# Kernel tuning notes

Measured on AMD Instinct MI355X. Metric: run time of the kernel, lower is better.

## Reference

```python
import jax, jax.numpy as jnp
import numpy as np

WH, WW = 8, 8            # window_size
NUM_HEADS = 8
DIM = 256
CPB_HIDDEN = 512
N = WH * WW


def _make_coords_table():
    # [1, 2*WH-1, 2*WW-1, 2] log-spaced continuous relative coords (Swin-V2)
    h = np.arange(-(WH - 1), WH, dtype=np.float32)
    w = np.arange(-(WW - 1), WW, dtype=np.float32)
    gh, gw = np.meshgrid(h, w, indexing='ij')
    table = np.stack([gh, gw], axis=-1)[None]  # [1,2WH-1,2WW-1,2]
    table[..., 0] /= (WH - 1)
    table[..., 1] /= (WW - 1)
    table *= 8.0
    table = np.sign(table) * np.log2(np.abs(table) + 1.0) / np.log2(8.0)
    return jnp.asarray(table, dtype=jnp.float32)


def _make_rel_pos_index():
    ch = np.arange(WH)
    cw = np.arange(WW)
    coords = np.stack(np.meshgrid(ch, cw, indexing='ij'))   # [2,WH,WW]
    cf = coords.reshape(2, -1)                               # [2,N]
    rel = cf[:, :, None] - cf[:, None, :]                    # [2,N,N]
    rel = rel.transpose(1, 2, 0).astype(np.int32)            # [N,N,2]
    rel[..., 0] += WH - 1
    rel[..., 1] += WW - 1
    rel[..., 0] *= 2 * WW - 1
    return jnp.asarray(rel.sum(-1), dtype=jnp.int32)         # [N,N]


def setup_inputs() -> dict:
    key = jax.random.key(0)
    ks = jax.random.split(key, 8)
    B_ = 2048
    nW = 64
    x = jax.random.normal(ks[0], (B_, N, DIM), dtype=jnp.float32)
    mask = jnp.zeros((nW, N, N), dtype=jnp.float32)
    qkv_w = jax.random.normal(ks[1], (3 * DIM, DIM), dtype=jnp.float32) * 0.02
    q_bias = jnp.zeros((DIM,), dtype=jnp.float32)
    v_bias = jnp.zeros((DIM,), dtype=jnp.float32)
    logit_scale = jnp.log(10.0 * jnp.ones((NUM_HEADS, 1, 1), dtype=jnp.float32))
    cpb_w1 = jax.random.normal(ks[2], (CPB_HIDDEN, 2), dtype=jnp.float32) * 0.02
    cpb_b1 = jnp.zeros((CPB_HIDDEN,), dtype=jnp.float32)
    cpb_w2 = jax.random.normal(ks[3], (NUM_HEADS, CPB_HIDDEN), dtype=jnp.float32) * 0.02
    proj_w = jax.random.normal(ks[4], (DIM, DIM), dtype=jnp.float32) * 0.02
    proj_b = jnp.zeros((DIM,), dtype=jnp.float32)
    return {
        'x': x, 'mask': mask,
        'qkv_w': qkv_w, 'q_bias': q_bias, 'v_bias': v_bias,
        'logit_scale': logit_scale,
        'cpb_w1': cpb_w1, 'cpb_b1': cpb_b1, 'cpb_w2': cpb_w2,
        'proj_w': proj_w, 'proj_b': proj_b,
        'coords_table': _make_coords_table(),
        'rel_idx': _make_rel_pos_index(),
    }


def reference(x, mask, qkv_w, q_bias, v_bias, logit_scale,
              cpb_w1, cpb_b1, cpb_w2, proj_w, proj_b,
              coords_table, rel_idx):
    B_, n, C = x.shape
    H = NUM_HEADS
    hd = C // H

    # qkv with [q_bias, 0, v_bias]
    qkv_bias = jnp.concatenate([q_bias, jnp.zeros_like(v_bias), v_bias])
    qkv = x @ qkv_w.T + qkv_bias                         # [B,N,3C]
    qkv = qkv.reshape(B_, n, 3, H, hd).transpose(2, 0, 3, 1, 4)
    q, k, v = qkv[0], qkv[1], qkv[2]                     # [B,H,N,hd]

    # cosine attention: L2-normalized q,k (eps as in F.normalize)
    qn = q / jnp.maximum(jnp.linalg.norm(q, axis=-1, keepdims=True), 1e-12)
    kn = k / jnp.maximum(jnp.linalg.norm(k, axis=-1, keepdims=True), 1e-12)
    attn = jnp.einsum('bhnd,bhmd->bhnm', qn, kn)         # [B,H,N,N]

    max_log = jnp.log(jnp.asarray(1.0 / 0.01, dtype=x.dtype))
    scale = jnp.exp(jnp.minimum(logit_scale, max_log))   # [H,1,1]
    attn = attn * scale

    # MLP relative position bias: 2 -> 512 -> H, gather, 16*sigmoid
    hid = jax.nn.relu(coords_table @ cpb_w1.T + cpb_b1)  # [1,2WH-1,2WW-1,512]
    table = (hid @ cpb_w2.T).reshape(-1, H)              # [(2WH-1)(2WW-1), H]
    bias = table[rel_idx.reshape(-1)].reshape(n, n, H)
    bias = 16.0 * jax.nn.sigmoid(bias.transpose(2, 0, 1))  # [H,N,N]
    attn = attn + bias[None]

    nW = mask.shape[0]
    attn = attn.reshape(B_ // nW, nW, H, n, n) + mask[None, :, None]
    attn = attn.reshape(B_, H, n, n)
    attn = jax.nn.softmax(attn, axis=-1)

    out = jnp.einsum('bhnm,bhmd->bhnd', attn, v)         # [B,H,N,hd]
    out = out.transpose(0, 2, 1, 3).reshape(B_, n, C)
    return out @ proj_w.T + proj_b
```

## Files before the change

### kernel.cpp

```cpp
#include <hip/hip_runtime.h>
#include <hip/hip_bf16.h>

typedef unsigned short u16;
typedef unsigned int   u32;
typedef __attribute__((ext_vector_type(8))) short short8;
typedef __attribute__((ext_vector_type(4))) short short4v;
typedef __attribute__((ext_vector_type(4))) float f32x4;

__device__ __forceinline__ u16 f2bf(float f) {
  u32 u = __float_as_uint(f);
  u32 r = (u + 0x7fffu + ((u >> 16) & 1u)) >> 16;
  return (u16)r;
}

__global__ __launch_bounds__(256) void wcvt_kernel(
    const float* __restrict__ qkvw, const float* __restrict__ pw,
    u16* __restrict__ wq, u16* __restrict__ wp) {
  const int e = (blockIdx.x * 256 + threadIdx.x) * 4;
  if (e < 196608) {
    const float4 v = *(const float4*)(qkvw + e);
    short4v o; o[0]=(short)f2bf(v.x); o[1]=(short)f2bf(v.y);
    o[2]=(short)f2bf(v.z); o[3]=(short)f2bf(v.w);
    *(short4v*)(wq + e) = o;
  } else {
    const int e2 = e - 196608;
    const float4 v = *(const float4*)(pw + e2);
    short4v o; o[0]=(short)f2bf(v.x); o[1]=(short)f2bf(v.y);
    o[2]=(short)f2bf(v.z); o[3]=(short)f2bf(v.w);
    *(short4v*)(wp + e2) = o;
  }
}

__global__ __launch_bounds__(256) void cpb_kernel(
    const float* __restrict__ ct, const float* __restrict__ w1,
    const float* __restrict__ b1, const float* __restrict__ w2,
    float* __restrict__ table) {
  const int r = blockIdx.x;
  const int t = threadIdx.x;
  const int lane = t & 63, wave = t >> 6;
  const float c0 = ct[r * 2 + 0];
  const float c1 = ct[r * 2 + 1];
  float acc[8] = {0.f, 0.f, 0.f, 0.f, 0.f, 0.f, 0.f, 0.f};
  for (int j = t; j < 512; j += 256) {
    float hid = fmaxf(c0 * w1[j * 2] + c1 * w1[j * 2 + 1] + b1[j], 0.f);
#pragma unroll
    for (int hh = 0; hh < 8; ++hh) acc[hh] += hid * w2[hh * 512 + j];
  }
#pragma unroll
  for (int hh = 0; hh < 8; ++hh)
#pragma unroll
    for (int off = 1; off < 64; off <<= 1) acc[hh] += __shfl_xor(acc[hh], off);
  __shared__ float red[4][8];
  if (lane == 0)
#pragma unroll
    for (int hh = 0; hh < 8; ++hh) red[wave][hh] = acc[hh];
  __syncthreads();
  if (t < 8) table[r * 8 + t] = red[0][t] + red[1][t] + red[2][t] + red[3][t];
}

__global__ __launch_bounds__(256) void bm_kernel(
    const float* __restrict__ table, const int* __restrict__ rel,
    const float* __restrict__ mask, float* __restrict__ bmP) {
  const int g = blockIdx.x * 256 + threadIdx.x;
  const int w = g >> 13;
  const int h = (g >> 10) & 7;
  const int m = (g >> 4) & 63;
  const int l = g & 15;
  float4 o;
#pragma unroll
  for (int j = 0; j < 4; ++j) {
    const int c = j * 16 + l;
    const float t = table[rel[m * 64 + c] * 8 + h];
    o[j] = 16.f / (1.f + __expf(-t)) + mask[(size_t)w * 4096 + m * 64 + c];
  }
  *(float4*)(bmP + ((((size_t)w * 8 + h) * 64 + m) * 64 + l * 4)) = o;
}

__global__ __launch_bounds__(512, 2) void fused_kernel(
    const float* __restrict__ X,
    const float* __restrict__ bmP,
    const float* __restrict__ lsc,
    const u16*  __restrict__ Wqb,
    const float* __restrict__ qb, const float* __restrict__ vbias,
    const u16*  __restrict__ Wpb,
    const float* __restrict__ pb,
    float* __restrict__ out) {
  __shared__ __attribute__((aligned(16))) u16 sA[16896];
  __shared__ __attribute__((aligned(16))) u16 sW[8][6912];

  const int bw = blockIdx.x;
  const int w  = bw & 63;
  const int tid  = threadIdx.x;
  const int wave = tid >> 6, lane = tid & 63;
  const int l15 = lane & 15, l4 = lane >> 4;
  const int h = wave;

  {
    const int cq  = tid & 7;
    const int rlo = tid >> 3;
    const float* xrow = X + ((size_t)bw * 64 + rlo) * 256;
#pragma unroll
    for (int kf = 0; kf < 8; ++kf) {
      const float4 xv = *(const float4*)(xrow + kf * 32 + cq * 4);
      short4v t4; t4[0]=(short)f2bf(xv.x); t4[1]=(short)f2bf(xv.y);
      t4[2]=(short)f2bf(xv.z); t4[3]=(short)f2bf(xv.w);
      *(short4v*)&sA[kf * 2048 + rlo * 32 + cq * 4] = t4;
    }
  }
  __syncthreads();

  u16* vt   = &sW[wave][0];
  u16* pbuf = &sW[wave][2304];

  f32x4 oa[4][2];

  {
    const int rb[6] = {h * 32, h * 32 + 16, 256 + h * 32, 256 + h * 32 + 16,
                       512 + h * 32, 512 + h * 32 + 16};
    f32x4 acc[4][6];
#pragma unroll
    for (int mi = 0; mi < 4; ++mi)
#pragma unroll
      for (int nj = 0; nj < 6; ++nj) acc[mi][nj] = (f32x4){0.f, 0.f, 0.f, 0.f};

    short8 bf_cur[6];
#pragma unroll
    for (int nj = 0; nj < 6; ++nj)
      bf_cur[nj] = *(const short8*)(Wqb + (size_t)(rb[nj] + l15) * 256 + l4 * 8);

#pragma unroll
    for (int kf = 0; kf < 8; ++kf) {
      short8 af[4];
#pragma unroll
      for (int mi = 0; mi < 4; ++mi)
        af[mi] = *(const short8*)&sA[kf * 2048 + (mi * 16 + l15) * 32 + l4 * 8];
      short8 bf_nxt[6];
      if (kf < 7) {
#pragma unroll
        for (int nj = 0; nj < 6; ++nj)
          bf_nxt[nj] = *(const short8*)(Wqb + (size_t)(rb[nj] + l15) * 256 + (kf + 1) * 32 + l4 * 8);
      }
#pragma unroll
      for (int nj = 0; nj < 6; ++nj)
#pragma unroll
        for (int mi = 0; mi < 4; ++mi)
          acc[mi][nj] = __builtin_amdgcn_mfma_f32_16x16x32_bf16(af[mi], bf_cur[nj], acc[mi][nj], 0, 0, 0);
      if (kf < 7) {
#pragma unroll
        for (int nj = 0; nj < 6; ++nj) bf_cur[nj] = bf_nxt[nj];
      }
    }

    u16* qstage = pbuf;
    u16* kstage = pbuf + 2048;
    {
      const float qb0 = qb[h * 32 + l15];
      const float qb1 = qb[h * 32 + 16 + l15];
#pragma unroll
      for (int mi = 0; mi < 4; ++mi)
#pragma unroll
        for (int r = 0; r < 4; ++r) {
          const float v0 = acc[mi][0][r] + qb0;
          const float v1 = acc[mi][1][r] + qb1;
          float ss = v0 * v0 + v1 * v1;
          ss += __shfl_xor(ss, 1); ss += __shfl_xor(ss, 2);
          ss += __shfl_xor(ss, 4); ss += __shfl_xor(ss, 8);
          const float inv = 1.f / fmaxf(sqrtf(ss), 1e-12f);
          const int m = mi * 16 + l4 * 4 + r;
          qstage[m * 32 + l15]      = f2bf(v0 * inv);
          qstage[m * 32 + 16 + l15] = f2bf(v1 * inv);
        }
#pragma unroll
      for (int mi = 0; mi < 4; ++mi)
#pragma unroll
        for (int r = 0; r < 4; ++r) {
          const float v0 = acc[mi][2][r];
          const float v1 = acc[mi][3][r];
          float ss = v0 * v0 + v1 * v1;
          ss += __shfl_xor(ss, 1); ss += __shfl_xor(ss, 2);
          ss += __shfl_xor(ss, 4); ss += __shfl_xor(ss, 8);
          const float inv = 1.f / fmaxf(sqrtf(ss), 1e-12f);
          const int m = mi * 16 + l4 * 4 + r;
          kstage[m * 32 + l15]      = f2bf(v0 * inv);
          kstage[m * 32 + 16 + l15] = f2bf(v1 * inv);
        }
      const float vb0 = vbias[h * 32 + l15];
      const float vb1 = vbias[h * 32 + 16 + l15];
#pragma unroll
      for (int mi = 0; mi < 4; ++mi)
#pragma unroll
        for (int r = 0; r < 4; ++r) {
          const int m = mi * 16 + l4 * 4 + r;
          vt[l15 * 72 + m]        = f2bf(acc[mi][4][r] + vb0);
          vt[(16 + l15) * 72 + m] = f2bf(acc[mi][5][r] + vb1);
        }
    }

    const float* bmbase = bmP + (((size_t)(w * 8 + h)) * 64) * 64 + l15 * 4;
    float4 bmv[4][4];
#pragma unroll
    for (int i = 0; i < 4; ++i)
#pragma unroll
      for (int r = 0; r < 4; ++r) {
        const int m = i * 16 + l4 * 4 + r;
        bmv[i][r] = *(const float4*)(bmbase + (size_t)m * 64);
      }

    short8 aq[4], bk[4];
#pragma unroll
    for (int i = 0; i < 4; ++i)
      aq[i] = *(const short8*)&qstage[(i * 16 + l15) * 32 + l4 * 8];
#pragma unroll
    for (int j = 0; j < 4; ++j)
      bk[j] = *(const short8*)&kstage[(j * 16 + l15) * 32 + l4 * 8];

    f32x4 s[4][4];
    __builtin_amdgcn_s_setprio(1);
#pragma unroll
    for (int i = 0; i < 4; ++i)
#pragma unroll
      for (int j = 0; j < 4; ++j) {
        const f32x4 z = {0.f, 0.f, 0.f, 0.f};
        s[i][j] = __builtin_amdgcn_mfma_f32_16x16x32_bf16(aq[i], bk[j], z, 0, 0, 0);
      }
    __builtin_amdgcn_s_setprio(0);

    const float scale = __expf(fminf(lsc[h], 4.60517018598809136804f));
    u16* pW = pbuf;

#pragma unroll
    for (int i = 0; i < 4; ++i)
#pragma unroll
      for (int r = 0; r < 4; ++r) {
        const int m = i * 16 + l4 * 4 + r;
        float v0[4]; float mx = -3.0e38f;
#pragma unroll
        for (int j = 0; j < 4; ++j) {
          const float sv = s[i][j][r] * scale + bmv[i][r][j];
          v0[j] = sv; mx = fmaxf(mx, sv);
        }
        mx = fmaxf(mx, __shfl_xor(mx, 1)); mx = fmaxf(mx, __shfl_xor(mx, 2));
        mx = fmaxf(mx, __shfl_xor(mx, 4)); mx = fmaxf(mx, __shfl_xor(mx, 8));
        float sum = 0.f;
#pragma unroll
        for (int j = 0; j < 4; ++j) { v0[j] = __expf(v0[j] - mx); sum += v0[j]; }
        sum += __shfl_xor(sum, 1); sum += __shfl_xor(sum, 2);
        sum += __shfl_xor(sum, 4); sum += __shfl_xor(sum, 8);
        const float isum = 1.f / sum;
#pragma unroll
        for (int j = 0; j < 4; ++j)
          pW[m * 72 + j * 16 + l15] = f2bf(v0[j] * isum);
      }

#pragma unroll
    for (int i = 0; i < 4; ++i)
#pragma unroll
      for (int nb = 0; nb < 2; ++nb) oa[i][nb] = (f32x4){0.f, 0.f, 0.f, 0.f};
#pragma unroll
    for (int kb = 0; kb < 2; ++kb) {
      short8 pa[4];
#pragma unroll
      for (int i = 0; i < 4; ++i)
        pa[i] = *(const short8*)&pW[(i * 16 + l15) * 72 + kb * 32 + l4 * 8];
      __builtin_amdgcn_s_setprio(1);
#pragma unroll
      for (int nb = 0; nb < 2; ++nb) {
        const short8 vb8 = *(const short8*)&vt[(nb * 16 + l15) * 72 + kb * 32 + l4 * 8];
#pragma unroll
        for (int i = 0; i < 4; ++i)
          oa[i][nb] = __builtin_amdgcn_mfma_f32_16x16x32_bf16(pa[i], vb8, oa[i][nb], 0, 0, 0);
      }
      __builtin_amdgcn_s_setprio(0);
    }
  }

  __syncthreads();

#pragma unroll
  for (int i = 0; i < 4; ++i)
#pragma unroll
    for (int nb = 0; nb < 2; ++nb)
#pragma unroll
      for (int r = 0; r < 4; ++r) {
        const int m = i * 16 + l4 * 4 + r;
        sA[m * 264 + h * 32 + nb * 16 + l15] = f2bf(oa[i][nb][r]);
      }
  __syncthreads();

  {
    const int n0 = wave * 32;
    const u16* pbase = Wpb + (size_t)(n0 + l15) * 256 + l4 * 8;
    f32x4 pacc[4][2];
#pragma unroll
    for (int mi = 0; mi < 4; ++mi)
#pragma unroll
      for (int nj = 0; nj < 2; ++nj) pacc[mi][nj] = (f32x4){0.f, 0.f, 0.f, 0.f};

    short8 bfr_cur[2];
#pragma unroll
    for (int nj = 0; nj < 2; ++nj)
      bfr_cur[nj] = *(const short8*)(pbase + (size_t)(nj * 16) * 256);

#pragma unroll
    for (int ks = 0; ks < 8; ++ks) {
      const int k0 = ks * 32;
      short8 afr[4];
#pragma unroll
      for (int mi = 0; mi < 4; ++mi)
        afr[mi] = *(const short8*)&sA[(mi * 16 + l15) * 264 + k0 + l4 * 8];
      short8 bfr_nxt[2];
      if (ks < 7) {
#pragma unroll
        for (int nj = 0; nj < 2; ++nj)
          bfr_nxt[nj] = *(const short8*)(pbase + (size_t)(nj * 16) * 256 + k0 + 32);
      }
#pragma unroll
      for (int nj = 0; nj < 2; ++nj)
#pragma unroll
        for (int mi = 0; mi < 4; ++mi)
          pacc[mi][nj] = __builtin_amdgcn_mfma_f32_16x16x32_bf16(afr[mi], bfr_cur[nj], pacc[mi][nj], 0, 0, 0);
      if (ks < 7) {
#pragma unroll
        for (int nj = 0; nj < 2; ++nj) bfr_cur[nj] = bfr_nxt[nj];
      }
    }
    float* orow = out + (size_t)bw * 64 * 256;
#pragma unroll
    for (int mi = 0; mi < 4; ++mi)
#pragma unroll
      for (int nj = 0; nj < 2; ++nj) {
        const int n = n0 + nj * 16 + l15;
        const float bias = pb[n];
#pragma unroll
        for (int r = 0; r < 4; ++r) {
          const int m = mi * 16 + l4 * 4 + r;
          orow[(size_t)m * 256 + n] = pacc[mi][nj][r] + bias;
        }
      }
  }
}

extern "C" void kernel_launch(void* const* d_in, const int* in_sizes, int n_in,
                              void* d_out, int out_size, void* d_ws, size_t ws_size,
                              hipStream_t stream) {
  (void)in_sizes; (void)n_in; (void)out_size; (void)ws_size;
  const float* x    = (const float*)d_in[0];
  const float* mask = (const float*)d_in[1];
  const float* qkvw = (const float*)d_in[2];
  const float* qb   = (const float*)d_in[3];
  const float* vb   = (const float*)d_in[4];
  const float* lsc  = (const float*)d_in[5];
  const float* w1   = (const float*)d_in[6];
  const float* b1   = (const float*)d_in[7];
  const float* w2   = (const float*)d_in[8];
  const float* pw   = (const float*)d_in[9];
  const float* pb   = (const float*)d_in[10];
  const float* ct   = (const float*)d_in[11];
  const int* rel    = (const int*)d_in[12];
  float* out = (float*)d_out;

  char* ws = (char*)d_ws;
  float* table = (float*)(ws);
  u16* Wqb = (u16*)(ws + 262144);
  u16* Wpb = (u16*)(ws + 720896);
  float* bmP = (float*)(ws + (1 << 20));

  wcvt_kernel<<<256, 256, 0, stream>>>(qkvw, pw, Wqb, Wpb);
  cpb_kernel<<<225, 256, 0, stream>>>(ct, w1, b1, w2, table);
  bm_kernel<<<2048, 256, 0, stream>>>(table, rel, mask, bmP);
  fused_kernel<<<2048, 512, 0, stream>>>(x, bmP, lsc, Wqb, qb, vb,
                                         Wpb, pb, out);
}
```

Before: 472.9 us.

## Split each head across two waves with 1024-thread blocks in fused attention

Doubles the fused kernel's block size to 1024 threads so two waves share each head. One wave computes Q plus half of V and the other computes K plus the other half, then each takes half the query rows for scores, softmax, PV and the output projection. The aim is to cut per-wave register pressure and serial work and raise parallelism per window. In exchange it adds block-wide barriers between phases, reuses the Q staging buffer for P, and drops the explicit two-blocks-per-CU occupancy hint.

```diff
diff --git a/kernel.cpp b/kernel.cpp
--- a/kernel.cpp
+++ b/kernel.cpp
@@ -76,7 +76,7 @@
   *(float4*)(bmP + ((((size_t)w * 8 + h) * 64 + m) * 64 + l * 4)) = o;
 }
 
-__global__ __launch_bounds__(512, 2) void fused_kernel(
+__global__ __launch_bounds__(1024) void fused_kernel(
     const float* __restrict__ X,
     const float* __restrict__ bmP,
     const float* __restrict__ lsc,
@@ -93,40 +93,48 @@
   const int tid  = threadIdx.x;
   const int wave = tid >> 6, lane = tid & 63;
   const int l15 = lane & 15, l4 = lane >> 4;
-  const int h = wave;
-
-  {
-    const int cq  = tid & 7;
-    const int rlo = tid >> 3;
-    const float* xrow = X + ((size_t)bw * 64 + rlo) * 256;
-#pragma unroll
-    for (int kf = 0; kf < 8; ++kf) {
-      const float4 xv = *(const float4*)(xrow + kf * 32 + cq * 4);
+  const int h    = wave >> 1;
+  const int half = wave & 1;
+
+  {
+    const int row = tid >> 4;
+    const int c4  = tid & 15;
+    const float* xrow = X + ((size_t)bw * 64 + row) * 256;
+#pragma unroll
+    for (int u = 0; u < 4; ++u) {
+      const int col = u * 64 + c4 * 4;
+      const int kf = col >> 5, co = col & 31;
+      const float4 xv = *(const float4*)(xrow + col);
       short4v t4; t4[0]=(short)f2bf(xv.x); t4[1]=(short)f2bf(xv.y);
       t4[2]=(short)f2bf(xv.z); t4[3]=(short)f2bf(xv.w);
-      *(short4v*)&sA[kf * 2048 + rlo * 32 + cq * 4] = t4;
-    }
-  }
-  __syncthreads();
-
-  u16* vt   = &sW[wave][0];
-  u16* pbuf = &sW[wave][2304];
-
-  f32x4 oa[4][2];
-
-  {
-    const int rb[6] = {h * 32, h * 32 + 16, 256 + h * 32, 256 + h * 32 + 16,
-                       512 + h * 32, 512 + h * 32 + 16};
-    f32x4 acc[4][6];
+      *(short4v*)&sA[kf * 2048 + row * 32 + co] = t4;
+    }
+  }
+  __syncthreads();
+
+  u16* vt = &sW[h][0];
+  u16* pq = &sW[h][2304];
+  u16* pk = &sW[h][4352];
+  u16* pP = &sW[h][2304];
+
+  {
+    const int rb0 = half ? (256 + h * 32)      : (h * 32);
+    const int rb1 = half ? (256 + h * 32 + 16) : (h * 32 + 16);
+    const int rb2 = half ? (512 + h * 32 + 16) : (512 + h * 32);
+    const u16* wb0 = Wqb + (size_t)(rb0 + l15) * 256 + l4 * 8;
+    const u16* wb1 = Wqb + (size_t)(rb1 + l15) * 256 + l4 * 8;
+    const u16* wb2 = Wqb + (size_t)(rb2 + l15) * 256 + l4 * 8;
+
+    f32x4 acc[4][3];
 #pragma unroll
     for (int mi = 0; mi < 4; ++mi)
 #pragma unroll
-      for (int nj = 0; nj < 6; ++nj) acc[mi][nj] = (f32x4){0.f, 0.f, 0.f, 0.f};
-
-    short8 bf_cur[6];
-#pragma unroll
-    for (int nj = 0; nj < 6; ++nj)
-      bf_cur[nj] = *(const short8*)(Wqb + (size_t)(rb[nj] + l15) * 256 + l4 * 8);
+      for (int nj = 0; nj < 3; ++nj) acc[mi][nj] = (f32x4){0.f, 0.f, 0.f, 0.f};
+
+    short8 bf_cur[3];
+    bf_cur[0] = *(const short8*)wb0;
+    bf_cur[1] = *(const short8*)wb1;
+    bf_cur[2] = *(const short8*)wb2;
 
 #pragma unroll
     for (int kf = 0; kf < 8; ++kf) {
@@ -134,105 +142,116 @@
 #pragma unroll
       for (int mi = 0; mi < 4; ++mi)
         af[mi] = *(const short8*)&sA[kf * 2048 + (mi * 16 + l15) * 32 + l4 * 8];
-      short8 bf_nxt[6];
+      short8 bf_nxt[3];
       if (kf < 7) {
-#pragma unroll
-        for (int nj = 0; nj < 6; ++nj)
-          bf_nxt[nj] = *(const short8*)(Wqb + (size_t)(rb[nj] + l15) * 256 + (kf + 1) * 32 + l4 * 8);
-      }
-#pragma unroll
-      for (int nj = 0; nj < 6; ++nj)
+        bf_nxt[0] = *(const short8*)(wb0 + (kf + 1) * 32);
+        bf_nxt[1] = *(const short8*)(wb1 + (kf + 1) * 32);
+        bf_nxt[2] = *(const short8*)(wb2 + (kf + 1) * 32);
+      }
+      __builtin_amdgcn_s_setprio(1);
+#pragma unroll
+      for (int nj = 0; nj < 3; ++nj)
 #pragma unroll
         for (int mi = 0; mi < 4; ++mi)
           acc[mi][nj] = __builtin_amdgcn_mfma_f32_16x16x32_bf16(af[mi], bf_cur[nj], acc[mi][nj], 0, 0, 0);
+      __builtin_amdgcn_s_setprio(0);
       if (kf < 7) {
 #pragma unroll
-        for (int nj = 0; nj < 6; ++nj) bf_cur[nj] = bf_nxt[nj];
-      }
-    }
-
-    u16* qstage = pbuf;
-    u16* kstage = pbuf + 2048;
-    {
-      const float qb0 = qb[h * 32 + l15];
-      const float qb1 = qb[h * 32 + 16 + l15];
-#pragma unroll
-      for (int mi = 0; mi < 4; ++mi)
-#pragma unroll
-        for (int r = 0; r < 4; ++r) {
-          const float v0 = acc[mi][0][r] + qb0;
-          const float v1 = acc[mi][1][r] + qb1;
+        for (int nj = 0; nj < 3; ++nj) bf_cur[nj] = bf_nxt[nj];
+      }
+    }
+
+    if (half == 0) {
+      const float b0 = qb[h * 32 + l15];
+      const float b1 = qb[h * 32 + 16 + l15];
+#pragma unroll
+      for (int mi = 0; mi < 4; ++mi)
+#pragma unroll
+        for (int r = 0; r < 4; ++r) {
+          const float v0 = acc[mi][0][r] + b0;
+          const float v1 = acc[mi][1][r] + b1;
           float ss = v0 * v0 + v1 * v1;
           ss += __shfl_xor(ss, 1); ss += __shfl_xor(ss, 2);
           ss += __shfl_xor(ss, 4); ss += __shfl_xor(ss, 8);
           const float inv = 1.f / fmaxf(sqrtf(ss), 1e-12f);
           const int m = mi * 16 + l4 * 4 + r;
-          qstage[m * 32 + l15]      = f2bf(v0 * inv);
-          qstage[m * 32 + 16 + l15] = f2bf(v1 * inv);
-        }
-#pragma unroll
-      for (int mi = 0; mi < 4; ++mi)
-#pragma unroll
-        for (int r = 0; r < 4; ++r) {
-          const float v0 = acc[mi][2][r];
-          const float v1 = acc[mi][3][r];
+          pq[m * 32 + l15]      = f2bf(v0 * inv);
+          pq[m * 32 + 16 + l15] = f2bf(v1 * inv);
+        }
+      const float vb0 = vbias[h * 32 + l15];
+#pragma unroll
+      for (int mi = 0; mi < 4; ++mi)
+#pragma unroll
+        for (int r = 0; r < 4; ++r) {
+          const int m = mi * 16 + l4 * 4 + r;
+          vt[l15 * 72 + m] = f2bf(acc[mi][2][r] + vb0);
+        }
+    } else {
+#pragma unroll
+      for (int mi = 0; mi < 4; ++mi)
+#pragma unroll
+        for (int r = 0; r < 4; ++r) {
+          const float v0 = acc[mi][0][r];
+          const float v1 = acc[mi][1][r];
           float ss = v0 * v0 + v1 * v1;
           ss += __shfl_xor(ss, 1); ss += __shfl_xor(ss, 2);
           ss += __shfl_xor(ss, 4); ss += __shfl_xor(ss, 8);
           const float inv = 1.f / fmaxf(sqrtf(ss), 1e-12f);
           const int m = mi * 16 + l4 * 4 + r;
-          kstage[m * 32 + l15]      = f2bf(v0 * inv);
-          kstage[m * 32 + 16 + l15] = f2bf(v1 * inv);
-        }
-      const float vb0 = vbias[h * 32 + l15];
+          pk[m * 32 + l15]      = f2bf(v0 * inv);
+          pk[m * 32 + 16 + l15] = f2bf(v1 * inv);
+        }
       const float vb1 = vbias[h * 32 + 16 + l15];
 #pragma unroll
       for (int mi = 0; mi < 4; ++mi)
 #pragma unroll
         for (int r = 0; r < 4; ++r) {
           const int m = mi * 16 + l4 * 4 + r;
-          vt[l15 * 72 + m]        = f2bf(acc[mi][4][r] + vb0);
-          vt[(16 + l15) * 72 + m] = f2bf(acc[mi][5][r] + vb1);
-        }
-    }
-
+          vt[(16 + l15) * 72 + m] = f2bf(acc[mi][2][r] + vb1);
+        }
+    }
+  }
+  __syncthreads();
+
+  f32x4 s[2][4];
+  float4 bmv[2][4];
+  {
     const float* bmbase = bmP + (((size_t)(w * 8 + h)) * 64) * 64 + l15 * 4;
-    float4 bmv[4][4];
-#pragma unroll
-    for (int i = 0; i < 4; ++i)
+#pragma unroll
+    for (int i = 0; i < 2; ++i)
 #pragma unroll
       for (int r = 0; r < 4; ++r) {
-        const int m = i * 16 + l4 * 4 + r;
+        const int m = half * 32 + i * 16 + l4 * 4 + r;
         bmv[i][r] = *(const float4*)(bmbase + (size_t)m * 64);
       }
 
-    short8 aq[4], bk[4];
-#pragma unroll
-    for (int i = 0; i < 4; ++i)
-      aq[i] = *(const short8*)&qstage[(i * 16 + l15) * 32 + l4 * 8];
+    short8 aq[2], bk[4];
+#pragma unroll
+    for (int i = 0; i < 2; ++i)
+      aq[i] = *(const short8*)&pq[(half * 32 + i * 16 + l15) * 32 + l4 * 8];
 #pragma unroll
     for (int j = 0; j < 4; ++j)
-      bk[j] = *(const short8*)&kstage[(j * 16 + l15) * 32 + l4 * 8];
-
-    f32x4 s[4][4];
+      bk[j] = *(const short8*)&pk[(j * 16 + l15) * 32 + l4 * 8];
+
     __builtin_amdgcn_s_setprio(1);
 #pragma unroll
-    for (int i = 0; i < 4; ++i)
+    for (int i = 0; i < 2; ++i)
 #pragma unroll
       for (int j = 0; j < 4; ++j) {
         const f32x4 z = {0.f, 0.f, 0.f, 0.f};
         s[i][j] = __builtin_amdgcn_mfma_f32_16x16x32_bf16(aq[i], bk[j], z, 0, 0, 0);
       }
     __builtin_amdgcn_s_setprio(0);
-
+  }
+  __syncthreads();
+
+  {
     const float scale = __expf(fminf(lsc[h], 4.60517018598809136804f));
-    u16* pW = pbuf;
-
-#pragma unroll
-    for (int i = 0; i < 4; ++i)
+#pragma unroll
+    for (int i = 0; i < 2; ++i)
 #pragma unroll
       for (int r = 0; r < 4; ++r) {
-        const int m = i * 16 + l4 * 4 + r;
+        const int prow = half * 32 + i * 16 + l4 * 4 + r;
         float v0[4]; float mx = -3.0e38f;
 #pragma unroll
         for (int j = 0; j < 4; ++j) {
@@ -249,50 +268,49 @@
         const float isum = 1.f / sum;
 #pragma unroll
         for (int j = 0; j < 4; ++j)
-          pW[m * 72 + j * 16 + l15] = f2bf(v0[j] * isum);
-      }
-
-#pragma unroll
-    for (int i = 0; i < 4; ++i)
+          pP[prow * 72 + j * 16 + l15] = f2bf(v0[j] * isum);
+      }
+
+    f32x4 oa[2][2];
+#pragma unroll
+    for (int i = 0; i < 2; ++i)
 #pragma unroll
       for (int nb = 0; nb < 2; ++nb) oa[i][nb] = (f32x4){0.f, 0.f, 0.f, 0.f};
 #pragma unroll
     for (int kb = 0; kb < 2; ++kb) {
-      short8 pa[4];
-#pragma unroll
-      for (int i = 0; i < 4; ++i)
-        pa[i] = *(const short8*)&pW[(i * 16 + l15) * 72 + kb * 32 + l4 * 8];
+      short8 pa[2];
+#pragma unroll
+      for (int i = 0; i < 2; ++i)
+        pa[i] = *(const short8*)&pP[(half * 32 + i * 16 + l15) * 72 + kb * 32 + l4 * 8];
       __builtin_amdgcn_s_setprio(1);
 #pragma unroll
       for (int nb = 0; nb < 2; ++nb) {
         const short8 vb8 = *(const short8*)&vt[(nb * 16 + l15) * 72 + kb * 32 + l4 * 8];
 #pragma unroll
-        for (int i = 0; i < 4; ++i)
+        for (int i = 0; i < 2; ++i)
           oa[i][nb] = __builtin_amdgcn_mfma_f32_16x16x32_bf16(pa[i], vb8, oa[i][nb], 0, 0, 0);
       }
       __builtin_amdgcn_s_setprio(0);
     }
-  }
-
-  __syncthreads();
-
-#pragma unroll
-  for (int i = 0; i < 4; ++i)
-#pragma unroll
-    for (int nb = 0; nb < 2; ++nb)
-#pragma unroll
-      for (int r = 0; r < 4; ++r) {
-        const int m = i * 16 + l4 * 4 + r;
-        sA[m * 264 + h * 32 + nb * 16 + l15] = f2bf(oa[i][nb][r]);
-      }
-  __syncthreads();
-
-  {
-    const int n0 = wave * 32;
+#pragma unroll
+    for (int i = 0; i < 2; ++i)
+#pragma unroll
+      for (int nb = 0; nb < 2; ++nb)
+#pragma unroll
+        for (int r = 0; r < 4; ++r) {
+          const int m = half * 32 + i * 16 + l4 * 4 + r;
+          sA[m * 264 + h * 32 + nb * 16 + l15] = f2bf(oa[i][nb][r]);
+        }
+  }
+  __syncthreads();
+
+  {
+    const int wm = wave & 1;
+    const int n0 = (wave >> 1) * 32;
     const u16* pbase = Wpb + (size_t)(n0 + l15) * 256 + l4 * 8;
-    f32x4 pacc[4][2];
-#pragma unroll
-    for (int mi = 0; mi < 4; ++mi)
+    f32x4 pacc[2][2];
+#pragma unroll
+    for (int mi = 0; mi < 2; ++mi)
 #pragma unroll
       for (int nj = 0; nj < 2; ++nj) pacc[mi][nj] = (f32x4){0.f, 0.f, 0.f, 0.f};
 
@@ -304,10 +322,10 @@
 #pragma unroll
     for (int ks = 0; ks < 8; ++ks) {
       const int k0 = ks * 32;
-      short8 afr[4];
-#pragma unroll
-      for (int mi = 0; mi < 4; ++mi)
-        afr[mi] = *(const short8*)&sA[(mi * 16 + l15) * 264 + k0 + l4 * 8];
+      short8 afr[2];
+#pragma unroll
+      for (int mi = 0; mi < 2; ++mi)
+        afr[mi] = *(const short8*)&sA[(wm * 32 + mi * 16 + l15) * 264 + k0 + l4 * 8];
       short8 bfr_nxt[2];
       if (ks < 7) {
 #pragma unroll
@@ -317,7 +335,7 @@
 #pragma unroll
       for (int nj = 0; nj < 2; ++nj)
 #pragma unroll
-        for (int mi = 0; mi < 4; ++mi)
+        for (int mi = 0; mi < 2; ++mi)
           pacc[mi][nj] = __builtin_amdgcn_mfma_f32_16x16x32_bf16(afr[mi], bfr_cur[nj], pacc[mi][nj], 0, 0, 0);
       if (ks < 7) {
 #pragma unroll
@@ -326,14 +344,14 @@
     }
     float* orow = out + (size_t)bw * 64 * 256;
 #pragma unroll
-    for (int mi = 0; mi < 4; ++mi)
+    for (int mi = 0; mi < 2; ++mi)
 #pragma unroll
       for (int nj = 0; nj < 2; ++nj) {
         const int n = n0 + nj * 16 + l15;
         const float bias = pb[n];
 #pragma unroll
         for (int r = 0; r < 4; ++r) {
-          const int m = mi * 16 + l4 * 4 + r;
+          const int m = wm * 32 + mi * 16 + l4 * 4 + r;
           orow[(size_t)m * 256 + n] = pacc[mi][nj][r] + bias;
         }
       }
@@ -368,6 +386,6 @@
   wcvt_kernel<<<256, 256, 0, stream>>>(qkvw, pw, Wqb, Wpb);
   cpb_kernel<<<225, 256, 0, stream>>>(ct, w1, b1, w2, table);
   bm_kernel<<<2048, 256, 0, stream>>>(table, rel, mask, bmP);
-  fused_kernel<<<2048, 512, 0, stream>>>(x, bmP, lsc, Wqb, qb, vb,
-                                         Wpb, pb, out);
-}
+  fused_kernel<<<2048, 1024, 0, stream>>>(x, bmP, lsc, Wqb, qb, vb,
+                                          Wpb, pb, out);
+}
```

Result: no change. 466.7 us (-1.3%).

## Split fused window attention into per-half-head attention and separate projection GEMM

Applied to the files above, without the earlier changes.

Replaces the single 512-thread fused kernel with two kernels. The first handles four heads per 256-thread block, loads X straight from global memory into MFMA fragments, and defers softmax normalisation to the output. The second is a tiled bf16 projection GEMM reading an intermediate O buffer held in workspace, and the work is chunked by workspace size. This removes the block-wide syncs and the large shared footprint to raise occupancy. In exchange, X is read twice (once per half block), the attention output makes an extra global round-trip in bf16, and more kernels are launched.

```diff
diff --git a/kernel.cpp b/kernel.cpp
--- a/kernel.cpp
+++ b/kernel.cpp
@@ -11,6 +11,12 @@
   u32 u = __float_as_uint(f);
   u32 r = (u + 0x7fffu + ((u >> 16) & 1u)) >> 16;
   return (u16)r;
+}
+__device__ __forceinline__ short8 cvt8(const float4 a, const float4 b) {
+  short8 o;
+  o[0]=(short)f2bf(a.x); o[1]=(short)f2bf(a.y); o[2]=(short)f2bf(a.z); o[3]=(short)f2bf(a.w);
+  o[4]=(short)f2bf(b.x); o[5]=(short)f2bf(b.y); o[6]=(short)f2bf(b.z); o[7]=(short)f2bf(b.w);
+  return o;
 }
 
 __global__ __launch_bounds__(256) void wcvt_kernel(
@@ -76,274 +82,234 @@
   *(float4*)(bmP + ((((size_t)w * 8 + h) * 64 + m) * 64 + l * 4)) = o;
 }
 
-__global__ __launch_bounds__(512, 2) void fused_kernel(
+__global__ __launch_bounds__(256, 3) void qkv_attn_kernel(
     const float* __restrict__ X,
     const float* __restrict__ bmP,
     const float* __restrict__ lsc,
     const u16*  __restrict__ Wqb,
     const float* __restrict__ qb, const float* __restrict__ vbias,
-    const u16*  __restrict__ Wpb,
-    const float* __restrict__ pb,
-    float* __restrict__ out) {
-  __shared__ __attribute__((aligned(16))) u16 sA[16896];
-  __shared__ __attribute__((aligned(16))) u16 sW[8][6912];
-
-  const int bw = blockIdx.x;
-  const int w  = bw & 63;
+    int win0,
+    u16* __restrict__ O) {
+  __shared__ __attribute__((aligned(16))) u16 sH[4][6528];
+
+  const int blk  = blockIdx.x;
+  const int bw   = win0 + (blk >> 1);
+  const int half = blk & 1;
   const int tid  = threadIdx.x;
   const int wave = tid >> 6, lane = tid & 63;
   const int l15 = lane & 15, l4 = lane >> 4;
-  const int h = wave;
+  const int h = half * 4 + wave;
+  const int w = bw & 63;
+
+  u16* vt = &sH[wave][0];
+  u16* pq = &sH[wave][2176];
+  u16* pk = &sH[wave][4352];
+  u16* pP = &sH[wave][2176];
+
+  const float* xbase = X + (size_t)(bw * 64) * 256;
+
+  f32x4 acc[4][6];
+#pragma unroll
+  for (int mi = 0; mi < 4; ++mi)
+#pragma unroll
+    for (int nj = 0; nj < 6; ++nj) acc[mi][nj] = (f32x4){0.f, 0.f, 0.f, 0.f};
+
+  const int rb[6] = {h * 32, h * 32 + 16, 256 + h * 32, 256 + h * 32 + 16,
+                     512 + h * 32, 512 + h * 32 + 16};
+#pragma unroll
+  for (int kf = 0; kf < 8; ++kf) {
+    short8 af[4];
+#pragma unroll
+    for (int mi = 0; mi < 4; ++mi) {
+      const float* xr = xbase + (size_t)(mi * 16 + l15) * 256 + kf * 32 + l4 * 8;
+      const float4 a0 = *(const float4*)(xr);
+      const float4 a1 = *(const float4*)(xr + 4);
+      af[mi] = cvt8(a0, a1);
+    }
+#pragma unroll
+    for (int nj = 0; nj < 6; ++nj) {
+      const short8 bf = *(const short8*)(
+          Wqb + (size_t)(rb[nj] + l15) * 256 + kf * 32 + l4 * 8);
+#pragma unroll
+      for (int mi = 0; mi < 4; ++mi)
+        acc[mi][nj] = __builtin_amdgcn_mfma_f32_16x16x32_bf16(af[mi], bf, acc[mi][nj], 0, 0, 0);
+    }
+  }
 
   {
-    const int cq  = tid & 7;
-    const int rlo = tid >> 3;
-    const float* xrow = X + ((size_t)bw * 64 + rlo) * 256;
-#pragma unroll
-    for (int kf = 0; kf < 8; ++kf) {
-      const float4 xv = *(const float4*)(xrow + kf * 32 + cq * 4);
-      short4v t4; t4[0]=(short)f2bf(xv.x); t4[1]=(short)f2bf(xv.y);
-      t4[2]=(short)f2bf(xv.z); t4[3]=(short)f2bf(xv.w);
-      *(short4v*)&sA[kf * 2048 + rlo * 32 + cq * 4] = t4;
-    }
-  }
-  __syncthreads();
-
-  u16* vt   = &sW[wave][0];
-  u16* pbuf = &sW[wave][2304];
+    const float qb0 = qb[h * 32 + l15];
+    const float qb1 = qb[h * 32 + 16 + l15];
+#pragma unroll
+    for (int mi = 0; mi < 4; ++mi)
+#pragma unroll
+      for (int r = 0; r < 4; ++r) {
+        const float v0 = acc[mi][0][r] + qb0;
+        const float v1 = acc[mi][1][r] + qb1;
+        float ss = v0 * v0 + v1 * v1;
+        ss += __shfl_xor(ss, 1); ss += __shfl_xor(ss, 2);
+        ss += __shfl_xor(ss, 4); ss += __shfl_xor(ss, 8);
+        const float inv = 1.f / fmaxf(sqrtf(ss), 1e-12f);
+        const int m = mi * 16 + l4 * 4 + r;
+        pq[m * 34 + l15]      = f2bf(v0 * inv);
+        pq[m * 34 + 16 + l15] = f2bf(v1 * inv);
+      }
+#pragma unroll
+    for (int mi = 0; mi < 4; ++mi)
+#pragma unroll
+      for (int r = 0; r < 4; ++r) {
+        const float v0 = acc[mi][2][r];
+        const float v1 = acc[mi][3][r];
+        float ss = v0 * v0 + v1 * v1;
+        ss += __shfl_xor(ss, 1); ss += __shfl_xor(ss, 2);
+        ss += __shfl_xor(ss, 4); ss += __shfl_xor(ss, 8);
+        const float inv = 1.f / fmaxf(sqrtf(ss), 1e-12f);
+        const int m = mi * 16 + l4 * 4 + r;
+        pk[m * 34 + l15]      = f2bf(v0 * inv);
+        pk[m * 34 + 16 + l15] = f2bf(v1 * inv);
+      }
+    const float vb0 = vbias[h * 32 + l15];
+    const float vb1 = vbias[h * 32 + 16 + l15];
+#pragma unroll
+    for (int mi = 0; mi < 4; ++mi)
+#pragma unroll
+      for (int r = 0; r < 4; ++r) {
+        const int m = mi * 16 + l4 * 4 + r;
+        vt[l15 * 68 + m]        = f2bf(acc[mi][4][r] + vb0);
+        vt[(16 + l15) * 68 + m] = f2bf(acc[mi][5][r] + vb1);
+      }
+  }
+
+  const float scale = __expf(fminf(lsc[h], 4.60517018598809136804f));
+  const float* bmbase = bmP + ((size_t)(w * 8 + h)) * 4096 + l15 * 4;
+  float is_[4][4];
+
+  short8 aq[4], bk[4];
+#pragma unroll
+  for (int j = 0; j < 4; ++j)
+    bk[j] = *(const short8*)&pk[(j * 16 + l15) * 34 + l4 * 8];
+#pragma unroll
+  for (int i = 0; i < 4; ++i)
+    aq[i] = *(const short8*)&pq[(i * 16 + l15) * 34 + l4 * 8];
+
+#pragma unroll
+  for (int i = 0; i < 4; ++i) {
+    float4 bmv[4];
+#pragma unroll
+    for (int r = 0; r < 4; ++r)
+      bmv[r] = *(const float4*)(bmbase + (size_t)(i * 16 + l4 * 4 + r) * 64);
+    f32x4 s4[4];
+    __builtin_amdgcn_s_setprio(1);
+#pragma unroll
+    for (int j = 0; j < 4; ++j) {
+      const f32x4 z = {0.f, 0.f, 0.f, 0.f};
+      s4[j] = __builtin_amdgcn_mfma_f32_16x16x32_bf16(aq[i], bk[j], z, 0, 0, 0);
+    }
+    __builtin_amdgcn_s_setprio(0);
+#pragma unroll
+    for (int r = 0; r < 4; ++r) {
+      const int m = i * 16 + l4 * 4 + r;
+      float v0[4]; float mx = -3.0e38f;
+#pragma unroll
+      for (int j = 0; j < 4; ++j) {
+        const float sv = s4[j][r] * scale + bmv[r][j];
+        v0[j] = sv; mx = fmaxf(mx, sv);
+      }
+      mx = fmaxf(mx, __shfl_xor(mx, 1)); mx = fmaxf(mx, __shfl_xor(mx, 2));
+      mx = fmaxf(mx, __shfl_xor(mx, 4)); mx = fmaxf(mx, __shfl_xor(mx, 8));
+      float sum = 0.f;
+#pragma unroll
+      for (int j = 0; j < 4; ++j) { v0[j] = __expf(v0[j] - mx); sum += v0[j]; }
+      sum += __shfl_xor(sum, 1); sum += __shfl_xor(sum, 2);
+      sum += __shfl_xor(sum, 4); sum += __shfl_xor(sum, 8);
+      is_[i][r] = 1.f / sum;
+#pragma unroll
+      for (int j = 0; j < 4; ++j)
+        pP[m * 68 + j * 16 + l15] = f2bf(v0[j]);
+    }
+  }
 
   f32x4 oa[4][2];
-
-  {
-    const int rb[6] = {h * 32, h * 32 + 16, 256 + h * 32, 256 + h * 32 + 16,
-                       512 + h * 32, 512 + h * 32 + 16};
-    f32x4 acc[4][6];
-#pragma unroll
-    for (int mi = 0; mi < 4; ++mi)
-#pragma unroll
-      for (int nj = 0; nj < 6; ++nj) acc[mi][nj] = (f32x4){0.f, 0.f, 0.f, 0.f};
-
-    short8 bf_cur[6];
-#pragma unroll
-    for (int nj = 0; nj < 6; ++nj)
-      bf_cur[nj] = *(const short8*)(Wqb + (size_t)(rb[nj] + l15) * 256 + l4 * 8);
-
-#pragma unroll
-    for (int kf = 0; kf < 8; ++kf) {
-      short8 af[4];
-#pragma unroll
-      for (int mi = 0; mi < 4; ++mi)
-        af[mi] = *(const short8*)&sA[kf * 2048 + (mi * 16 + l15) * 32 + l4 * 8];
-      short8 bf_nxt[6];
-      if (kf < 7) {
-#pragma unroll
-        for (int nj = 0; nj < 6; ++nj)
-          bf_nxt[nj] = *(const short8*)(Wqb + (size_t)(rb[nj] + l15) * 256 + (kf + 1) * 32 + l4 * 8);
-      }
-#pragma unroll
-      for (int nj = 0; nj < 6; ++nj)
-#pragma unroll
-        for (int mi = 0; mi < 4; ++mi)
-          acc[mi][nj] = __builtin_amdgcn_mfma_f32_16x16x32_bf16(af[mi], bf_cur[nj], acc[mi][nj], 0, 0, 0);
-      if (kf < 7) {
-#pragma unroll
-        for (int nj = 0; nj < 6; ++nj) bf_cur[nj] = bf_nxt[nj];
-      }
-    }
-
-    u16* qstage = pbuf;
-    u16* kstage = pbuf + 2048;
-    {
-      const float qb0 = qb[h * 32 + l15];
-      const float qb1 = qb[h * 32 + 16 + l15];
-#pragma unroll
-      for (int mi = 0; mi < 4; ++mi)
-#pragma unroll
-        for (int r = 0; r < 4; ++r) {
-          const float v0 = acc[mi][0][r] + qb0;
-          const float v1 = acc[mi][1][r] + qb1;
-          float ss = v0 * v0 + v1 * v1;
-          ss += __shfl_xor(ss, 1); ss += __shfl_xor(ss, 2);
-          ss += __shfl_xor(ss, 4); ss += __shfl_xor(ss, 8);
-          const float inv = 1.f / fmaxf(sqrtf(ss), 1e-12f);
-          const int m = mi * 16 + l4 * 4 + r;
-          qstage[m * 32 + l15]      = f2bf(v0 * inv);
-          qstage[m * 32 + 16 + l15] = f2bf(v1 * inv);
-        }
-#pragma unroll
-      for (int mi = 0; mi < 4; ++mi)
-#pragma unroll
-        for (int r = 0; r < 4; ++r) {
-          const float v0 = acc[mi][2][r];
-          const float v1 = acc[mi][3][r];
-          float ss = v0 * v0 + v1 * v1;
-          ss += __shfl_xor(ss, 1); ss += __shfl_xor(ss, 2);
-          ss += __shfl_xor(ss, 4); ss += __shfl_xor(ss, 8);
-          const float inv = 1.f / fmaxf(sqrtf(ss), 1e-12f);
-          const int m = mi * 16 + l4 * 4 + r;
-          kstage[m * 32 + l15]      = f2bf(v0 * inv);
-          kstage[m * 32 + 16 + l15] = f2bf(v1 * inv);
-        }
-      const float vb0 = vbias[h * 32 + l15];
-      const float vb1 = vbias[h * 32 + 16 + l15];
-#pragma unroll
-      for (int mi = 0; mi < 4; ++mi)
-#pragma unroll
-        for (int r = 0; r < 4; ++r) {
-          const int m = mi * 16 + l4 * 4 + r;
-          vt[l15 * 72 + m]        = f2bf(acc[mi][4][r] + vb0);
-          vt[(16 + l15) * 72 + m] = f2bf(acc[mi][5][r] + vb1);
-        }
-    }
-
-    const float* bmbase = bmP + (((size_t)(w * 8 + h)) * 64) * 64 + l15 * 4;
-    float4 bmv[4][4];
+#pragma unroll
+  for (int i = 0; i < 4; ++i)
+#pragma unroll
+    for (int nb = 0; nb < 2; ++nb) oa[i][nb] = (f32x4){0.f, 0.f, 0.f, 0.f};
+#pragma unroll
+  for (int kb = 0; kb < 2; ++kb) {
+    short8 pa[4];
 #pragma unroll
     for (int i = 0; i < 4; ++i)
+      pa[i] = *(const short8*)&pP[(i * 16 + l15) * 68 + kb * 32 + l4 * 8];
+    __builtin_amdgcn_s_setprio(1);
+#pragma unroll
+    for (int nb = 0; nb < 2; ++nb) {
+      const short8 vb8 = *(const short8*)&vt[(nb * 16 + l15) * 68 + kb * 32 + l4 * 8];
+#pragma unroll
+      for (int i = 0; i < 4; ++i)
+        oa[i][nb] = __builtin_amdgcn_mfma_f32_16x16x32_bf16(pa[i], vb8, oa[i][nb], 0, 0, 0);
+    }
+    __builtin_amdgcn_s_setprio(0);
+  }
+
+  u16* obase = O + ((size_t)(blk >> 1) * 64) * 256 + h * 32;
+#pragma unroll
+  for (int i = 0; i < 4; ++i)
+#pragma unroll
+    for (int nb = 0; nb < 2; ++nb)
 #pragma unroll
       for (int r = 0; r < 4; ++r) {
         const int m = i * 16 + l4 * 4 + r;
-        bmv[i][r] = *(const float4*)(bmbase + (size_t)m * 64);
-      }
-
-    short8 aq[4], bk[4];
-#pragma unroll
-    for (int i = 0; i < 4; ++i)
-      aq[i] = *(const short8*)&qstage[(i * 16 + l15) * 32 + l4 * 8];
-#pragma unroll
-    for (int j = 0; j < 4; ++j)
-      bk[j] = *(const short8*)&kstage[(j * 16 + l15) * 32 + l4 * 8];
-
-    f32x4 s[4][4];
-    __builtin_amdgcn_s_setprio(1);
-#pragma unroll
-    for (int i = 0; i < 4; ++i)
-#pragma unroll
-      for (int j = 0; j < 4; ++j) {
-        const f32x4 z = {0.f, 0.f, 0.f, 0.f};
-        s[i][j] = __builtin_amdgcn_mfma_f32_16x16x32_bf16(aq[i], bk[j], z, 0, 0, 0);
-      }
-    __builtin_amdgcn_s_setprio(0);
-
-    const float scale = __expf(fminf(lsc[h], 4.60517018598809136804f));
-    u16* pW = pbuf;
-
-#pragma unroll
-    for (int i = 0; i < 4; ++i)
-#pragma unroll
-      for (int r = 0; r < 4; ++r) {
-        const int m = i * 16 + l4 * 4 + r;
-        float v0[4]; float mx = -3.0e38f;
-#pragma unroll
-        for (int j = 0; j < 4; ++j) {
-          const float sv = s[i][j][r] * scale + bmv[i][r][j];
-          v0[j] = sv; mx = fmaxf(mx, sv);
-        }
-        mx = fmaxf(mx, __shfl_xor(mx, 1)); mx = fmaxf(mx, __shfl_xor(mx, 2));
-        mx = fmaxf(mx, __shfl_xor(mx, 4)); mx = fmaxf(mx, __shfl_xor(mx, 8));
-        float sum = 0.f;
-#pragma unroll
-        for (int j = 0; j < 4; ++j) { v0[j] = __expf(v0[j] - mx); sum += v0[j]; }
-        sum += __shfl_xor(sum, 1); sum += __shfl_xor(sum, 2);
-        sum += __shfl_xor(sum, 4); sum += __shfl_xor(sum, 8);
-        const float isum = 1.f / sum;
-#pragma unroll
-        for (int j = 0; j < 4; ++j)
-          pW[m * 72 + j * 16 + l15] = f2bf(v0[j] * isum);
-      }
-
-#pragma unroll
-    for (int i = 0; i < 4; ++i)
-#pragma unroll
-      for (int nb = 0; nb < 2; ++nb) oa[i][nb] = (f32x4){0.f, 0.f, 0.f, 0.f};
-#pragma unroll
-    for (int kb = 0; kb < 2; ++kb) {
-      short8 pa[4];
-#pragma unroll
-      for (int i = 0; i < 4; ++i)
-        pa[i] = *(const short8*)&pW[(i * 16 + l15) * 72 + kb * 32 + l4 * 8];
-      __builtin_amdgcn_s_setprio(1);
-#pragma unroll
-      for (int nb = 0; nb < 2; ++nb) {
-        const short8 vb8 = *(const short8*)&vt[(nb * 16 + l15) * 72 + kb * 32 + l4 * 8];
-#pragma unroll
-        for (int i = 0; i < 4; ++i)
-          oa[i][nb] = __builtin_amdgcn_mfma_f32_16x16x32_bf16(pa[i], vb8, oa[i][nb], 0, 0, 0);
-      }
-      __builtin_amdgcn_s_setprio(0);
-    }
-  }
-
-  __syncthreads();
-
-#pragma unroll
-  for (int i = 0; i < 4; ++i)
-#pragma unroll
-    for (int nb = 0; nb < 2; ++nb)
-#pragma unroll
-      for (int r = 0; r < 4; ++r) {
-        const int m = i * 16 + l4 * 4 + r;
-        sA[m * 264 + h * 32 + nb * 16 + l15] = f2bf(oa[i][nb][r]);
-      }
-  __syncthreads();
-
-  {
-    const int n0 = wave * 32;
-    const u16* pbase = Wpb + (size_t)(n0 + l15) * 256 + l4 * 8;
-    f32x4 pacc[4][2];
-#pragma unroll
-    for (int mi = 0; mi < 4; ++mi)
-#pragma unroll
-      for (int nj = 0; nj < 2; ++nj) pacc[mi][nj] = (f32x4){0.f, 0.f, 0.f, 0.f};
-
-    short8 bfr_cur[2];
-#pragma unroll
-    for (int nj = 0; nj < 2; ++nj)
-      bfr_cur[nj] = *(const short8*)(pbase + (size_t)(nj * 16) * 256);
-
-#pragma unroll
-    for (int ks = 0; ks < 8; ++ks) {
-      const int k0 = ks * 32;
-      short8 afr[4];
-#pragma unroll
-      for (int mi = 0; mi < 4; ++mi)
-        afr[mi] = *(const short8*)&sA[(mi * 16 + l15) * 264 + k0 + l4 * 8];
-      short8 bfr_nxt[2];
-      if (ks < 7) {
-#pragma unroll
-        for (int nj = 0; nj < 2; ++nj)
-          bfr_nxt[nj] = *(const short8*)(pbase + (size_t)(nj * 16) * 256 + k0 + 32);
-      }
-#pragma unroll
-      for (int nj = 0; nj < 2; ++nj)
-#pragma unroll
-        for (int mi = 0; mi < 4; ++mi)
-          pacc[mi][nj] = __builtin_amdgcn_mfma_f32_16x16x32_bf16(afr[mi], bfr_cur[nj], pacc[mi][nj], 0, 0, 0);
-      if (ks < 7) {
-#pragma unroll
-        for (int nj = 0; nj < 2; ++nj) bfr_cur[nj] = bfr_nxt[nj];
-      }
-    }
-    float* orow = out + (size_t)bw * 64 * 256;
-#pragma unroll
-    for (int mi = 0; mi < 4; ++mi)
-#pragma unroll
-      for (int nj = 0; nj < 2; ++nj) {
-        const int n = n0 + nj * 16 + l15;
-        const float bias = pb[n];
-#pragma unroll
-        for (int r = 0; r < 4; ++r) {
-          const int m = mi * 16 + l4 * 4 + r;
-          orow[(size_t)m * 256 + n] = pacc[mi][nj][r] + bias;
-        }
-      }
-  }
+        obase[(size_t)m * 256 + nb * 16 + l15] = f2bf(oa[i][nb][r] * is_[i][r]);
+      }
+}
+
+__global__ __launch_bounds__(256) void proj_kernel(
+    const u16* __restrict__ O, const u16* __restrict__ Wpb,
+    const float* __restrict__ pb, float* __restrict__ out) {
+  const int tid = threadIdx.x;
+  const int wave = tid >> 6, lane = tid & 63;
+  const int l15 = lane & 15, l4 = lane >> 4;
+  const int mt = blockIdx.x >> 1, nt = blockIdx.x & 1;
+  const int m0 = mt * 128 + wave * 32;
+  const int n0 = nt * 128;
+
+  const u16* ab = O + (size_t)(m0 + l15) * 256 + l4 * 8;
+  f32x4 acc[2][8];
+#pragma unroll
+  for (int mi = 0; mi < 2; ++mi)
+#pragma unroll
+    for (int nj = 0; nj < 8; ++nj) acc[mi][nj] = (f32x4){0.f, 0.f, 0.f, 0.f};
+
+#pragma unroll
+  for (int kf = 0; kf < 8; ++kf) {
+    short8 af[2];
+    af[0] = *(const short8*)(ab + kf * 32);
+    af[1] = *(const short8*)(ab + (size_t)16 * 256 + kf * 32);
+#pragma unroll
+    for (int nj = 0; nj < 8; ++nj) {
+      const short8 bf = *(const short8*)(
+          Wpb + (size_t)(n0 + nj * 16 + l15) * 256 + kf * 32 + l4 * 8);
+      acc[0][nj] = __builtin_amdgcn_mfma_f32_16x16x32_bf16(af[0], bf, acc[0][nj], 0, 0, 0);
+      acc[1][nj] = __builtin_amdgcn_mfma_f32_16x16x32_bf16(af[1], bf, acc[1][nj], 0, 0, 0);
+    }
+  }
+#pragma unroll
+  for (int mi = 0; mi < 2; ++mi)
+#pragma unroll
+    for (int nj = 0; nj < 8; ++nj) {
+      const int n = n0 + nj * 16 + l15;
+      const float bias = pb[n];
+#pragma unroll
+      for (int r = 0; r < 4; ++r) {
+        const int m = m0 + mi * 16 + l4 * 4 + r;
+        out[(size_t)m * 256 + n] = acc[mi][nj][r] + bias;
+      }
+    }
 }
 
 extern "C" void kernel_launch(void* const* d_in, const int* in_sizes, int n_in,
                               void* d_out, int out_size, void* d_ws, size_t ws_size,
                               hipStream_t stream) {
-  (void)in_sizes; (void)n_in; (void)out_size; (void)ws_size;
+  (void)in_sizes; (void)n_in; (void)out_size;
   const float* x    = (const float*)d_in[0];
   const float* mask = (const float*)d_in[1];
   const float* qkvw = (const float*)d_in[2];
@@ -364,10 +330,22 @@
   u16* Wqb = (u16*)(ws + 262144);
   u16* Wpb = (u16*)(ws + 720896);
   float* bmP = (float*)(ws + (1 << 20));
+  u16* O = (u16*)(ws + (16u << 20));
+
+  int nch = 8;
+  for (int c = 1; c <= 8; c <<= 1) {
+    if (ws_size >= (size_t)(16u << 20) + 67108864ull / c) { nch = c; break; }
+  }
+  const int CHUNK_WIN = 2048 / nch;
 
   wcvt_kernel<<<256, 256, 0, stream>>>(qkvw, pw, Wqb, Wpb);
   cpb_kernel<<<225, 256, 0, stream>>>(ct, w1, b1, w2, table);
   bm_kernel<<<2048, 256, 0, stream>>>(table, rel, mask, bmP);
-  fused_kernel<<<2048, 512, 0, stream>>>(x, bmP, lsc, Wqb, qb, vb,
-                                         Wpb, pb, out);
-}
+
+  for (int c = 0; c < nch; ++c) {
+    qkv_attn_kernel<<<CHUNK_WIN * 2, 256, 0, stream>>>(
+        x, bmP, lsc, Wqb, qb, vb, c * CHUNK_WIN, O);
+    proj_kernel<<<CHUNK_WIN, 256, 0, stream>>>(
+        O, Wpb, pb, out + (size_t)c * CHUNK_WIN * 64 * 256);
+  }
+}
```

After: 644.6 us. +36.3%, slower.
